# Optimization experiments

Measured on AMD Instinct MI355X. Metric: run time of the kernel, lower is better.

The kernel has to match this reference:

```python
import jax, jax.numpy as jnp
import numpy as np

CONF_THRES = 0.5   # self.conf_thres
NMS_THRES = 0.5    # self.nms_thres
PRE_NMS = 2048     # candidates kept before pairwise IoU
MAX_DET = 300      # padded detections returned per image
MAX_WH = 4096.0    # class-offset trick so NMS is per-class
IMG_SIZE = 416.0   # self.img_size; boxes_scale (416,416)->(416,416) => scale 1


def xywh2xyxy(b):
    xy, wh = b[..., :2], b[..., 2:4]
    return jnp.concatenate([xy - wh * 0.5, xy + wh * 0.5], axis=-1)


def pairwise_iou(boxes):
    # boxes: [K,4] xyxy -> [K,K] IoU
    area = (boxes[:, 2] - boxes[:, 0]) * (boxes[:, 3] - boxes[:, 1])
    lt = jnp.maximum(boxes[:, None, :2], boxes[None, :, :2])
    rb = jnp.minimum(boxes[:, None, 2:], boxes[None, :, 2:])
    wh = jnp.clip(rb - lt, 0.0)
    inter = wh[..., 0] * wh[..., 1]
    return inter / (area[:, None] + area[None, :] - inter + 1e-16)


def nms_single(pred):
    # pred: [N,85] = xywh(4) + objectness(1) + class scores(80)
    boxes = xywh2xyxy(pred[:, :4])
    obj = pred[:, 4]
    cls_scores = pred[:, 5:] * obj[:, None]        # conf = obj * class prob
    conf = jnp.max(cls_scores, axis=-1)
    cls_id = jnp.argmax(cls_scores, axis=-1)
    valid = obj >= CONF_THRES                      # confidence threshold filter
    score = jnp.where(valid, conf, -1.0)

    order = jnp.argsort(-score)[:PRE_NMS]          # sort desc, keep top PRE_NMS
    boxes_s = boxes[order]
    score_s = score[order]
    cls_s = cls_id[order]
    valid_s = valid[order]

    # per-class NMS via coordinate offset by class id
    off = cls_s.astype(boxes_s.dtype) * MAX_WH
    iou = pairwise_iou(boxes_s + off[:, None])     # [PRE_NMS, PRE_NMS]

    def body(keep, i):
        suppressed = jnp.any(keep & (iou[:, i] > NMS_THRES))
        k = valid_s[i] & ~suppressed
        return keep.at[i].set(k), k

    keep, _ = jax.lax.scan(body, jnp.zeros(PRE_NMS, dtype=bool), jnp.arange(PRE_NMS))

    final_score = jnp.where(keep, score_s, -1.0)
    top = jnp.argsort(-final_score)[:MAX_DET]
    kb, ks, kc, km = boxes_s[top], score_s[top], cls_s[top], keep[top]

    scale = IMG_SIZE / 416.0                       # boxes_scale (identity here)
    det = jnp.concatenate(
        [kb * scale, ks[:, None], kc[:, None].astype(kb.dtype)], axis=-1)
    return jnp.where(km[:, None], det, 0.0)        # [MAX_DET, 6] padded


def setup_inputs() -> dict:
    key = jax.random.key(0)
    predictions = jax.random.uniform(key, (16, 10647, 85), dtype=jnp.float32)
    return {"predictions": predictions}


def reference(predictions):
    # detections per image: [x1,y1,x2,y2,score,class], zero-padded to MAX_DET
    return jax.vmap(nms_single)(predictions)  # [B, MAX_DET, 6]
```

## Files before the change

### kernel.cpp

```cpp
#include <hip/hip_runtime.h>
#include <hip/hip_bf16.h>
#include <stdint.h>

typedef unsigned long long u64;
typedef unsigned int u32;
typedef unsigned short u16;

#define NANCH 10647
#define NBATCH 16
#define NSORT 16384
#define NSEL 2048
#define NWORD 32
#define NCLS 80
#define CONF_T 0.5f
#define NMS_T 0.5f
#define MAXDET 300
#define MAXWH 4096.0f
#define CANDCAP 10688
#define PART 1344
#define NBLK1 84

__device__ __forceinline__ float dec_score(u64 key) {
    u32 v = ~(u32)(key >> 32);
    u32 u = (v & 0x80000000u) ? (v & 0x7FFFFFFFu) : ~v;
    return __uint_as_float(u);
}

__global__ __launch_bounds__(256) void k_prep(const float* __restrict__ pred,
                                              u64* __restrict__ keys,
                                              float4* __restrict__ boxes,
                                              int* __restrict__ cls,
                                              u32* __restrict__ bhist) {
    __shared__ float sm[128 * 85];
    __shared__ u32 ph[256];
    int b = blockIdx.y;
    int a0 = blockIdx.x * 128;
    int na = NANCH - a0; if (na > 128) na = 128;
    const float* src = pred + ((size_t)b * NANCH + a0) * 85;
    int tot = na * 85;
    ph[threadIdx.x] = 0;
    {
        size_t srcaddr = (size_t)src;
        int shift = (int)((srcaddr & 15) >> 2);
        const float4* A = (const float4*)(srcaddr & ~(size_t)15);
        int nvec = (tot + shift + 3) >> 2;
        for (int j = threadIdx.x; j < nvec; j += 256) {
            float4 v = A[j];
            int base = 4 * j - shift;
            if (base >= 0 && base + 3 < tot) {
                sm[base] = v.x; sm[base + 1] = v.y;
                sm[base + 2] = v.z; sm[base + 3] = v.w;
            } else {
                if (base >= 0 && base < tot)         sm[base]     = v.x;
                if (base + 1 >= 0 && base + 1 < tot) sm[base + 1] = v.y;
                if (base + 2 >= 0 && base + 2 < tot) sm[base + 2] = v.z;
                if (base + 3 >= 0 && base + 3 < tot) sm[base + 3] = v.w;
            }
        }
    }
    __syncthreads();
    int t = threadIdx.x;
    u64 kk = 0;
    if (t < na) {
        const float* s = &sm[t * 85];
        float x = s[0], y = s[1], w = s[2], h = s[3], obj = s[4];
        float best = s[5] * obj; int arg = 0;
        #pragma unroll
        for (int c = 1; c < 80; ++c) {
            float v = s[5 + c] * obj;
            if (v > best) { best = v; arg = c; }
        }
        bool valid = obj >= CONF_T;
        float sc = valid ? best : -1.0f;
        int a = a0 + t;
        float4 bx;
        bx.x = x - w * 0.5f; bx.y = y - h * 0.5f;
        bx.z = x + w * 0.5f; bx.w = y + h * 0.5f;
        size_t o = (size_t)b * NANCH + a;
        boxes[o] = bx;
        cls[o] = arg;
        u32 u = __float_as_uint(sc);
        u32 v = (u & 0x80000000u) ? ~u : (u | 0x80000000u);
        u32 hi = ~v;
        kk = ((u64)hi << 32) | (u32)a;
        keys[(size_t)b * NSORT + a] = kk;
    }
    u32 bin = (t < na) ? (u32)(kk >> 56) : 0xFFFFFFFFu;
    int lane = t & 63;
    u64 rem = __ballot(t < na);
    while (rem) {
        int srcl = __ffsll((long long)rem) - 1;
        u32 lb = __shfl(bin, srcl);
        u64 same = __ballot(bin == lb) & rem;
        if (lane == srcl) atomicAdd(&ph[lb], (u32)__popcll(same));
        rem &= ~same;
    }
    __syncthreads();
    bhist[(((size_t)b * NBLK1) + blockIdx.x) * 256 + threadIdx.x] = ph[threadIdx.x];
}

__global__ __launch_bounds__(1024) void k_scan(const u64* __restrict__ keys,
                                               const u32* __restrict__ bhist,
                                               u64* __restrict__ gslice,
                                               uint2* __restrict__ gpart) {
    __shared__ u32 hist[256];
    __shared__ u32 hsc[256];
    __shared__ u32 s_D0;
    __shared__ u32 wcs[16], wcc[16];
    __shared__ u32 s_tc;
    int b = blockIdx.y;
    int part = blockIdx.x;
    int tid = threadIdx.x;
    int lane = tid & 63, wv = tid >> 6;
    u64 below = (1ULL << lane) - 1ULL;
    const u64* KB = keys + (size_t)b * NSORT;

    if (tid < 256) {
        u32 h = 0;
        const u32* BH = bhist + (size_t)b * NBLK1 * 256 + tid;
        for (int j = 0; j < NBLK1; ++j) h += BH[(size_t)j * 256];
        hist[tid] = h;
    }
    __syncthreads();
    if (tid < 64) {
        u32 h0 = hist[tid*4], h1 = hist[tid*4+1], h2 = hist[tid*4+2], h3 = hist[tid*4+3];
        u32 loc = h0 + h1 + h2 + h3;
        u32 p = loc;
        #pragma unroll
        for (int o = 1; o < 64; o <<= 1) { u32 t2 = __shfl_up(p, o); if (lane >= o) p += t2; }
        u32 base = p - loc;
        hsc[tid*4]   = base + h0;
        hsc[tid*4+1] = base + h0 + h1;
        hsc[tid*4+2] = base + h0 + h1 + h2;
        hsc[tid*4+3] = base + h0 + h1 + h2 + h3;
    }
    __syncthreads();
    if (tid < 256) {
        u32 inc = hsc[tid], cb = inc - hist[tid];
        if (cb < NSEL && NSEL <= inc) s_D0 = tid;
    }
    __syncthreads();
    u32 D0 = s_D0;

    u64 kk0 = 0, kk1 = 0;
    bool s0 = false, s1 = false, c0 = false, c1 = false;
    {
        int off = tid, i = part * PART + off;
        bool inb = (off < PART) && (i < NANCH);
        kk0 = inb ? KB[i] : 0ULL;
        u32 top = (u32)(kk0 >> 56);
        s0 = inb && (top < D0); c0 = inb && (top == D0);
    }
    {
        int off = 1024 + tid, i = part * PART + off;
        bool inb = (off < PART) && (i < NANCH);
        kk1 = inb ? KB[i] : 0ULL;
        u32 top = (u32)(kk1 >> 56);
        s1 = inb && (top < D0); c1 = inb && (top == D0);
    }
    u64 bs0 = __ballot(s0), bs1 = __ballot(s1);
    u64 bc0 = __ballot(c0), bc1 = __ballot(c1);
    if (lane == 0) {
        wcs[wv] = (u32)(__popcll(bs0) + __popcll(bs1));
        wcc[wv] = (u32)(__popcll(bc0) + __popcll(bc1));
    }
    __syncthreads();
    if (tid < 16) {
        u32 vs = wcs[tid], vc = wcc[tid];
        u32 ps = vs, pc = vc;
        #pragma unroll
        for (int o = 1; o < 16; o <<= 1) {
            u32 ts = __shfl_up(ps, o);
            u32 tc = __shfl_up(pc, o);
            if (tid >= o) { ps += ts; pc += tc; }
        }
        wcs[tid] = ps - vs;
        wcc[tid] = pc - vc;
        if (tid == 15) {
            s_tc = pc;
            gpart[(size_t)b * 8 + part] = make_uint2(ps, pc);
        }
    }
    __syncthreads();
    u64* SL = gslice + ((size_t)b * 8 + part) * (size_t)PART;
    u32 base_s = wcs[wv];
    u32 base_c = (u32)PART - s_tc + wcc[wv];
    if (s0) SL[base_s + __popcll(bs0 & below)] = kk0;
    if (s1) SL[base_s + __popcll(bs0) + __popcll(bs1 & below)] = kk1;
    if (c0) SL[base_c + __popcll(bc0 & below)] = kk0;
    if (c1) SL[base_c + __popcll(bc0) + __popcll(bc1 & below)] = kk1;
}

__global__ __launch_bounds__(1024) void k_fin(const u64* __restrict__ gslice,
                                              const uint2* __restrict__ gpart,
                                              u64* __restrict__ gskey,
                                              u64* __restrict__ gkeep) {
    __shared__ u64 sk[NSEL];
    __shared__ u64 cand[CANDCAP];
    __shared__ u32 hist[256];
    __shared__ u32 hsc[256];
    __shared__ u64 s_red[16];
    __shared__ u32 ssA[8], ccA[8], soff[9], coff[9];
    __shared__ u32 s_D, s_rank, s_cnt, s_cand;

    int b = blockIdx.x;
    int tid = threadIdx.x;
    int lane = tid & 63;
    u64 below = (1ULL << lane) - 1ULL;

    if (tid < 8) { uint2 v = gpart[(size_t)b * 8 + tid]; ssA[tid] = v.x; ccA[tid] = v.y; }
    for (int i = tid; i < NSEL; i += 1024) sk[i] = ~0ULL;
    __syncthreads();
    if (tid == 0) {
        u32 a = 0, c2 = 0;
        for (int j = 0; j < 8; ++j) { soff[j] = a; a += ssA[j]; coff[j] = c2; c2 += ccA[j]; }
        soff[8] = a; coff[8] = c2;
        s_cnt = a; s_rank = NSEL - a; s_cand = c2;
    }
    __syncthreads();
    for (int j = 0; j < 8; ++j) {
        const u64* SL = gslice + ((size_t)b * 8 + j) * (size_t)PART;
        u32 ns = ssA[j], nc = ccA[j];
        u32 so = soff[j], co = coff[j];
        for (u32 i = tid; i < ns; i += 1024) sk[so + i] = SL[i];
        for (u32 i = tid; i < nc; i += 1024) cand[co + i] = SL[PART - nc + i];
    }
    __syncthreads();

    const int shifts2[5] = {48, 40, 32, 8, 0};
    for (int rr = 0; ; ++rr) {
        u32 cn = s_cand, r = s_rank;
        if (r == cn || rr == 5) {
            for (u32 i0 = 0; i0 < cn; i0 += 1024) {
                u32 i = i0 + tid;
                bool take = i < cn;
                u64 kk = take ? cand[i] : 0ULL;
                u64 bt = __ballot(take);
                u32 base = 0;
                if (lane == 0 && bt) base = atomicAdd(&s_cnt, (u32)__popcll(bt));
                base = __shfl(base, 0);
                if (take) sk[base + __popcll(bt & below)] = kk;
            }
            break;
        }
        if (r == 1) {
            u64 best = ~0ULL;
            for (u32 i = tid; i < cn; i += 1024) { u64 kk = cand[i]; if (kk < best) best = kk; }
            #pragma unroll
            for (int o = 32; o > 0; o >>= 1) {
                u64 other = __shfl_down(best, o);
                if (other < best) best = other;
            }
            if (lane == 0) s_red[tid >> 6] = best;
            __syncthreads();
            if (tid == 0) {
                u64 m = s_red[0];
                for (int w2 = 1; w2 < 16; ++w2) if (s_red[w2] < m) m = s_red[w2];
                sk[atomicAdd(&s_cnt, 1u)] = m;
            }
            break;
        }
        int shift = shifts2[rr];
        if (tid < 256) hist[tid] = 0;
        __syncthreads();
        for (u32 i = tid; i < cn; i += 1024)
            atomicAdd(&hist[(u32)(cand[i] >> shift) & 0xFFu], 1u);
        __syncthreads();
        if (tid < 64) {
            u32 h0 = hist[tid*4], h1 = hist[tid*4+1], h2 = hist[tid*4+2], h3 = hist[tid*4+3];
            u32 loc = h0 + h1 + h2 + h3;
            u32 p = loc;
            #pragma unroll
            for (int o = 1; o < 64; o <<= 1) { u32 t2 = __shfl_up(p, o); if (lane >= o) p += t2; }
            u32 base = p - loc;
            hsc[tid*4]   = base + h0;
            hsc[tid*4+1] = base + h0 + h1;
            hsc[tid*4+2] = base + h0 + h1 + h2;
            hsc[tid*4+3] = base + h0 + h1 + h2 + h3;
        }
        __syncthreads();
        if (tid < 256) {
            u32 inc = hsc[tid], cb = inc - hist[tid];
            if (cb < r && r <= inc) { s_D = tid; s_rank = r - cb; }
        }
        __syncthreads();
        u32 D = s_D;
        u64 vv[11]; bool vb[11];
        #pragma unroll
        for (int it = 0; it < 11; ++it) {
            u32 i = tid + it * 1024;
            vb[it] = (i < cn);
            vv[it] = vb[it] ? cand[i] : 0ULL;
        }
        __syncthreads();
        if (tid == 0) s_cand = 0;
        __syncthreads();
        #pragma unroll
        for (int it = 0; it < 11; ++it) {
            u32 dg = (u32)(vv[it] >> shift) & 0xFFu;
            bool tk = vb[it] && (dg < D);
            u64 bt = __ballot(tk);
            u32 base = 0;
            if (lane == 0 && bt) base = atomicAdd(&s_cnt, (u32)__popcll(bt));
            base = __shfl(base, 0);
            if (tk) sk[base + __popcll(bt & below)] = vv[it];
        }
        #pragma unroll
        for (int it = 0; it < 11; ++it) {
            u32 dg = (u32)(vv[it] >> shift) & 0xFFu;
            bool tk = vb[it] && (dg == D);
            u64 bt = __ballot(tk);
            u32 base = 0;
            if (lane == 0 && bt) base = atomicAdd(&s_cand, (u32)__popcll(bt));
            base = __shfl(base, 0);
            if (tk) cand[base + __popcll(bt & below)] = vv[it];
        }
        __syncthreads();
    }
    __syncthreads();

    {
        int w = tid >> 6, l = lane;
        int base = w * 128;
        u64 a = sk[base + l], c = sk[base + 64 + l];
        #pragma unroll
        for (int k = 2; k <= 128; k <<= 1) {
            for (int j = k >> 1; j > 0; j >>= 1) {
                if (j == 64) {
                    bool dir = (((base + l) & k) == 0);
                    u64 lo = a < c ? a : c;
                    u64 hi = a < c ? c : a;
                    a = dir ? lo : hi;
                    c = dir ? hi : lo;
                } else {
                    bool up_ = (l & j) != 0;
                    bool dira = (((base + l) & k) == 0);
                    bool dirc = (((base + 64 + l) & k) == 0);
                    u64 pa = __shfl_xor(a, j);
                    u64 pc = __shfl_xor(c, j);
                    a = (up_ == dira) ? (a > pa ? a : pa) : (a < pa ? a : pa);
                    c = (up_ == dirc) ? (c > pc ? c : pc) : (c < pc ? c : pc);
                }
            }
        }
        sk[base + l] = a; sk[base + 64 + l] = c;
        __syncthreads();
        for (int k = 256; k <= NSEL; k <<= 1) {
            for (int j = k >> 1; j >= 128; j >>= 1) {
                int n = tid;
                int i = ((n & ~(j - 1)) << 1) | (n & (j - 1));
                int l2 = i | j;
                u64 x = sk[i], y = sk[l2];
                bool up2 = ((i & k) == 0);
                if ((x > y) == up2) { sk[i] = y; sk[l2] = x; }
                __syncthreads();
            }
            a = sk[base + l]; c = sk[base + 64 + l];
            bool dirk = ((base & k) == 0);
            {
                u64 lo = a < c ? a : c;
                u64 hi = a < c ? c : a;
                a = dirk ? lo : hi;
                c = dirk ? hi : lo;
            }
            #pragma unroll
            for (int j = 32; j > 0; j >>= 1) {
                bool up_ = (l & j) != 0;
                u64 pa = __shfl_xor(a, j);
                u64 pc = __shfl_xor(c, j);
                a = (up_ == dirk) ? (a > pa ? a : pa) : (a < pa ? a : pa);
                c = (up_ == dirk) ? (c > pc ? c : pc) : (c < pc ? c : pc);
            }
            sk[base + l] = a; sk[base + 64 + l] = c;
            __syncthreads();
        }
    }

    for (int i = tid; i < NSEL; i += 1024) gskey[(size_t)b * NSEL + i] = sk[i];
    if (tid < NWORD) gkeep[(size_t)b * NWORD + tid] = 0ULL;
}

__global__ __launch_bounds__(256) void k_gather(const u64* __restrict__ gskey,
                                                const float4* __restrict__ boxes,
                                                const int* __restrict__ cls,
                                                float4* __restrict__ sel_box,
                                                float4* __restrict__ sel_sbox,
                                                float* __restrict__ sel_area,
                                                float* __restrict__ sel_score,
                                                int* __restrict__ sel_cls) {
    int b = blockIdx.y;
    int r = blockIdx.x * 256 + threadIdx.x;
    u64 key = gskey[(size_t)b * NSEL + r];
    int a = (int)(key & 0xFFFFFFFFu);
    if ((unsigned)a >= NANCH) a = 0;
    size_t src = (size_t)b * NANCH + a;
    float4 bx = boxes[src];
    int c = cls[src];
    float sc = dec_score(key);
    float off = (float)c * MAXWH;
    float4 sb;
    sb.x = bx.x + off; sb.y = bx.y + off;
    sb.z = bx.z + off; sb.w = bx.w + off;
    float area = (sb.z - sb.x) * (sb.w - sb.y);
    size_t o = (size_t)b * NSEL + r;
    sel_box[o] = bx; sel_sbox[o] = sb; sel_area[o] = area;
    sel_score[o] = sc; sel_cls[o] = c;
}

__global__ __launch_bounds__(1024) void k_cnms(const float4* __restrict__ sel_sbox,
                                               const float* __restrict__ sel_area,
                                               const int* __restrict__ sel_cls,
                                               const float* __restrict__ sel_score,
                                               u64* __restrict__ gkeep) {
    __shared__ u16 wmem[16][NSEL];
    __shared__ u64 wkeep[16][NWORD];

    int b = blockIdx.y;
    int cg = blockIdx.x;
    int lane = threadIdx.x & 63, wv = threadIdx.x >> 6;
    int c = cg * 16 + wv;
    size_t bb = (size_t)b * NSEL;
    const int* CL = sel_cls + bb;
    const float* SC = sel_score + bb;
    u64 below = (1ULL << lane) - 1ULL;

    int n = 0;
    for (int ch = 0; ch < NWORD; ++ch) {
        int i = ch * 64 + lane;
        bool pred = (CL[i] == c) && (SC[i] >= 0.0f);
        u64 bal = __ballot(pred);
        if (pred) wmem[wv][n + __popcll(bal & below)] = (u16)i;
        n += __popcll(bal);
    }

    for (int c0 = 0; c0 < n; c0 += 64) {
        int chunkn = n - c0; if (chunkn > 64) chunkn = 64;
        bool mv = lane < chunkn;
        int q = mv ? (int)wmem[wv][c0 + lane] : 0;
        float4 bq = sel_sbox[bb + q];
        float aq = sel_area[bb + q];

        bool hit = false;
        for (int j = 0; j < c0; ++j) {
            if (!((wkeep[wv][j >> 6] >> (j & 63)) & 1ULL)) continue;
            int p = (int)wmem[wv][j];
            float4 bp = sel_sbox[bb + p];
            float ap = sel_area[bb + p];
            float ltx = fmaxf(bp.x, bq.x), lty = fmaxf(bp.y, bq.y);
            float rbx = fminf(bp.z, bq.z), rby = fminf(bp.w, bq.w);
            float ww = fmaxf(rbx - ltx, 0.0f), hh = fmaxf(rby - lty, 0.0f);
            float inter = ww * hh;
            hit = hit || (mv && (inter / (ap + aq - inter + 1e-16f) > NMS_T));
        }
        u64 avail = __ballot(mv && !hit);

        u64 Rt = 0;
        for (int t = 0; t < chunkn; ++t) {
            int p = (int)wmem[wv][c0 + t];
            float4 bp = sel_sbox[bb + p];
            float ap = sel_area[bb + p];
            float ltx = fmaxf(bp.x, bq.x), lty = fmaxf(bp.y, bq.y);
            float rbx = fminf(bp.z, bq.z), rby = fminf(bp.w, bq.w);
            float ww = fmaxf(rbx - ltx, 0.0f), hh = fmaxf(rby - lty, 0.0f);
            float inter = ww * hh;
            u64 row = __ballot(mv && (inter / (ap + aq - inter + 1e-16f) > NMS_T));
            if (lane == t) Rt = row;
        }

        u64 U = avail, kept = 0;
        while (U) {
            bool inU = ((U >> lane) & 1ULL) != 0ULL;
            u64 newk = __ballot(inU && ((Rt & U & below) == 0ULL));
            u64 killed = __ballot((Rt & newk) != 0ULL);
            kept |= newk;
            U &= ~(newk | killed);
        }
        if (lane == 0) wkeep[wv][c0 >> 6] = kept;
        if ((kept >> lane) & 1ULL)
            atomicOr(&gkeep[(size_t)b * NWORD + (q >> 6)], 1ULL << (q & 63));
    }
}

__global__ __launch_bounds__(64) void k_out(const u64* __restrict__ gkeep,
                                            const float4* __restrict__ sel_box,
                                            const float* __restrict__ sel_score,
                                            const int* __restrict__ sel_cls,
                                            float* __restrict__ out) {
    int b = blockIdx.x;
    int lane = threadIdx.x;
    const float* SC = sel_score + (size_t)b * NSEL;
    u64 kreg = (lane < NWORD) ? gkeep[(size_t)b * NWORD + lane] : 0ULL;

    int cnt = (lane < NWORD) ? __popcll(kreg) : 0;
    int pre = cnt;
    #pragma unroll
    for (int dd = 1; dd < 64; dd <<= 1) {
        int o = __shfl_up(pre, dd);
        if (lane >= dd) pre += o;
    }
    int total = __shfl(pre, 63);
    int base = pre - cnt;
    float* OUT = out + (size_t)b * MAXDET * 6;
    if (lane < NWORD) {
        u64 m = kreg;
        int rr = 0;
        while (m) {
            int t = __ffsll((long long)m) - 1;
            m &= m - 1;
            int slot = base + rr; ++rr;
            if (slot < MAXDET) {
                int i = lane * 64 + t;
                size_t src = (size_t)b * NSEL + i;
                float4 bx = sel_box[src];
                float sc = SC[i];
                int c = sel_cls[src];
                float* o6 = OUT + slot * 6;
                o6[0] = bx.x; o6[1] = bx.y; o6[2] = bx.z; o6[3] = bx.w;
                o6[4] = sc; o6[5] = (float)c;
            }
        }
    }
    int start = total > MAXDET ? MAXDET : total;
    for (int s = start + lane; s < MAXDET; s += 64) {
        float* o6 = OUT + s * 6;
        o6[0] = 0.0f; o6[1] = 0.0f; o6[2] = 0.0f;
        o6[3] = 0.0f; o6[4] = 0.0f; o6[5] = 0.0f;
    }
}

extern "C" void kernel_launch(void* const* d_in, const int* in_sizes, int n_in,
                              void* d_out, int out_size, void* d_ws, size_t ws_size,
                              hipStream_t stream) {
    const float* pred = (const float*)d_in[0];
    float* out = (float*)d_out;

    char* ws = (char*)d_ws;
    size_t off = 0;
    auto alloc = [&](size_t bytes) -> void* {
        void* p = ws + off;
        off += (bytes + 255) & ~(size_t)255;
        return p;
    };

    u64*    keys      = (u64*)   alloc((size_t)NBATCH * NSORT * 8);
    float4* boxes     = (float4*)alloc((size_t)NBATCH * NANCH * 16);
    int*    cls       = (int*)   alloc((size_t)NBATCH * NANCH * 4);
    u32*    bhist     = (u32*)   alloc((size_t)NBATCH * NBLK1 * 256 * 4);
    u64*    gslice    = (u64*)   alloc((size_t)NBATCH * 8 * PART * 8);
    uint2*  gpart     = (uint2*) alloc((size_t)NBATCH * 8 * 8);
    u64*    gskey     = (u64*)   alloc((size_t)NBATCH * NSEL * 8);
    u64*    gkeep     = (u64*)   alloc((size_t)NBATCH * NWORD * 8);
    float4* sel_box   = (float4*)alloc((size_t)NBATCH * NSEL * 16);
    float4* sel_sbox  = (float4*)alloc((size_t)NBATCH * NSEL * 16);
    float*  sel_area  = (float*) alloc((size_t)NBATCH * NSEL * 4);
    float*  sel_score = (float*) alloc((size_t)NBATCH * NSEL * 4);
    int*    sel_cls   = (int*)   alloc((size_t)NBATCH * NSEL * 4);

    dim3 g1(NBLK1, NBATCH);
    k_prep<<<g1, 256, 0, stream>>>(pred, keys, boxes, cls, bhist);

    dim3 g2(8, NBATCH);
    k_scan<<<g2, 1024, 0, stream>>>(keys, bhist, gslice, gpart);

    k_fin<<<NBATCH, 1024, 0, stream>>>(gslice, gpart, gskey, gkeep);

    dim3 g4(8, NBATCH);
    k_gather<<<g4, 256, 0, stream>>>(gskey, boxes, cls,
                                     sel_box, sel_sbox, sel_area,
                                     sel_score, sel_cls);

    dim3 g5(5, NBATCH);
    k_cnms<<<g5, 1024, 0, stream>>>(sel_sbox, sel_area, sel_cls, sel_score, gkeep);

    k_out<<<NBATCH, 64, 0, stream>>>(gkeep, sel_box, sel_score, sel_cls, out);
}
```

Before: 103.0 us.

## Fuse second radix-select digit histogram into scan kernel and parallelize slice compaction

The scan kernel now also builds a histogram of the second key byte for the boundary-bucket candidates and accumulates it globally with atomics, zeroed in the prep kernel. The final kernel uses that histogram to resolve the second digit up front, so its first radix refinement round over the candidates is skipped. Slice copying is also spread across waves, with one wave per slice for selected keys and one per slice for candidates, using atomic offsets instead of serial per-slice loops. The cost is extra shared and global atomics in the scan kernel, and zeroing ghist2 in k_prep relies on kernel ordering on the stream.

```diff
diff --git a/kernel.cpp b/kernel.cpp
--- a/kernel.cpp
+++ b/kernel.cpp
@@ -30,10 +30,12 @@
                                               u64* __restrict__ keys,
                                               float4* __restrict__ boxes,
                                               int* __restrict__ cls,
-                                              u32* __restrict__ bhist) {
+                                              u32* __restrict__ bhist,
+                                              u32* __restrict__ ghist2) {
     __shared__ float sm[128 * 85];
     __shared__ u32 ph[256];
     int b = blockIdx.y;
+    if (blockIdx.x == 0) ghist2[(size_t)b * 256 + threadIdx.x] = 0;
     int a0 = blockIdx.x * 128;
     int na = NANCH - a0; if (na > 128) na = 128;
     const float* src = pred + ((size_t)b * NANCH + a0) * 85;
@@ -102,9 +104,11 @@
 __global__ __launch_bounds__(1024) void k_scan(const u64* __restrict__ keys,
                                                const u32* __restrict__ bhist,
                                                u64* __restrict__ gslice,
-                                               uint2* __restrict__ gpart) {
+                                               uint2* __restrict__ gpart,
+                                               u32* __restrict__ ghist2) {
     __shared__ u32 hist[256];
     __shared__ u32 hsc[256];
+    __shared__ u32 ph2[256];
     __shared__ u32 s_D0;
     __shared__ u32 wcs[16], wcc[16];
     __shared__ u32 s_tc;
@@ -116,6 +120,7 @@
     const u64* KB = keys + (size_t)b * NSORT;
 
     if (tid < 256) {
+        ph2[tid] = 0;
         u32 h = 0;
         const u32* BH = bhist + (size_t)b * NBLK1 * 256 + tid;
         for (int j = 0; j < NBLK1; ++j) h += BH[(size_t)j * 256];
@@ -158,6 +163,8 @@
         u32 top = (u32)(kk1 >> 56);
         s1 = inb && (top < D0); c1 = inb && (top == D0);
     }
+    if (c0) atomicAdd(&ph2[(u32)(kk0 >> 48) & 0xFFu], 1u);
+    if (c1) atomicAdd(&ph2[(u32)(kk1 >> 48) & 0xFFu], 1u);
     u64 bs0 = __ballot(s0), bs1 = __ballot(s1);
     u64 bc0 = __ballot(c0), bc1 = __ballot(c1);
     if (lane == 0) {
@@ -189,10 +196,12 @@
     if (s1) SL[base_s + __popcll(bs0) + __popcll(bs1 & below)] = kk1;
     if (c0) SL[base_c + __popcll(bc0 & below)] = kk0;
     if (c1) SL[base_c + __popcll(bc0) + __popcll(bc1 & below)] = kk1;
+    if (tid < 256 && ph2[tid]) atomicAdd(&ghist2[(size_t)b * 256 + tid], ph2[tid]);
 }
 
 __global__ __launch_bounds__(1024) void k_fin(const u64* __restrict__ gslice,
                                               const uint2* __restrict__ gpart,
+                                              const u32* __restrict__ ghist2,
                                               u64* __restrict__ gskey,
                                               u64* __restrict__ gkeep) {
     __shared__ u64 sk[NSEL];
@@ -200,35 +209,87 @@
     __shared__ u32 hist[256];
     __shared__ u32 hsc[256];
     __shared__ u64 s_red[16];
-    __shared__ u32 ssA[8], ccA[8], soff[9], coff[9];
-    __shared__ u32 s_D, s_rank, s_cnt, s_cand;
+    __shared__ u32 ssA[8], ccA[8];
+    __shared__ u32 s_D, s_r0, s_rank, s_cnt, s_cand;
 
     int b = blockIdx.x;
     int tid = threadIdx.x;
-    int lane = tid & 63;
+    int lane = tid & 63, wv = tid >> 6;
     u64 below = (1ULL << lane) - 1ULL;
 
     if (tid < 8) { uint2 v = gpart[(size_t)b * 8 + tid]; ssA[tid] = v.x; ccA[tid] = v.y; }
+    if (tid < 256) hist[tid] = ghist2[(size_t)b * 256 + tid];
     for (int i = tid; i < NSEL; i += 1024) sk[i] = ~0ULL;
     __syncthreads();
     if (tid == 0) {
-        u32 a = 0, c2 = 0;
-        for (int j = 0; j < 8; ++j) { soff[j] = a; a += ssA[j]; coff[j] = c2; c2 += ccA[j]; }
-        soff[8] = a; coff[8] = c2;
-        s_cnt = a; s_rank = NSEL - a; s_cand = c2;
-    }
-    __syncthreads();
-    for (int j = 0; j < 8; ++j) {
+        u32 a = 0;
+        for (int j = 0; j < 8; ++j) a += ssA[j];
+        s_r0 = NSEL - a;
+        s_cnt = 0; s_cand = 0;
+    }
+    if (tid < 64) {
+        u32 h0 = hist[tid*4], h1 = hist[tid*4+1], h2 = hist[tid*4+2], h3 = hist[tid*4+3];
+        u32 loc = h0 + h1 + h2 + h3;
+        u32 p = loc;
+        #pragma unroll
+        for (int o = 1; o < 64; o <<= 1) { u32 t2 = __shfl_up(p, o); if (lane >= o) p += t2; }
+        u32 base = p - loc;
+        hsc[tid*4]   = base + h0;
+        hsc[tid*4+1] = base + h0 + h1;
+        hsc[tid*4+2] = base + h0 + h1 + h2;
+        hsc[tid*4+3] = base + h0 + h1 + h2 + h3;
+    }
+    __syncthreads();
+    if (tid < 256) {
+        u32 inc = hsc[tid], cb = inc - hist[tid];
+        u32 r0 = s_r0;
+        if (cb < r0 && r0 <= inc) s_D = tid;
+    }
+    __syncthreads();
+    u32 D48 = s_D;
+
+    if (wv < 8) {
+        int j = wv;
         const u64* SL = gslice + ((size_t)b * 8 + j) * (size_t)PART;
-        u32 ns = ssA[j], nc = ccA[j];
-        u32 so = soff[j], co = coff[j];
-        for (u32 i = tid; i < ns; i += 1024) sk[so + i] = SL[i];
-        for (u32 i = tid; i < nc; i += 1024) cand[co + i] = SL[PART - nc + i];
-    }
+        u32 ns = ssA[j];
+        for (u32 i0 = 0; i0 < ns; i0 += 64) {
+            u32 i = i0 + lane;
+            bool act = i < ns;
+            u64 kk = act ? SL[i] : 0ULL;
+            u64 bal = __ballot(act);
+            u32 base = 0;
+            if (lane == 0) base = atomicAdd(&s_cnt, (u32)__popcll(bal));
+            base = __shfl(base, 0);
+            if (act) sk[base + __popcll(bal & below)] = kk;
+        }
+    } else {
+        int j = wv - 8;
+        u32 nc = ccA[j];
+        const u64* SL = gslice + ((size_t)b * 8 + j) * (size_t)PART + (PART - nc);
+        for (u32 i0 = 0; i0 < nc; i0 += 64) {
+            u32 i = i0 + lane;
+            bool act = i < nc;
+            u64 kk = act ? SL[i] : 0ULL;
+            u32 dg = (u32)(kk >> 48) & 0xFFu;
+            bool tks = act && (dg < D48);
+            bool tkc = act && (dg == D48);
+            u64 bs = __ballot(tks), bc = __ballot(tkc);
+            u32 base_s = 0, base_c = 0;
+            if (lane == 0) {
+                if (bs) base_s = atomicAdd(&s_cnt, (u32)__popcll(bs));
+                if (bc) base_c = atomicAdd(&s_cand, (u32)__popcll(bc));
+            }
+            base_s = __shfl(base_s, 0); base_c = __shfl(base_c, 0);
+            if (tks) sk[base_s + __popcll(bs & below)] = kk;
+            if (tkc) cand[base_c + __popcll(bc & below)] = kk;
+        }
+    }
+    __syncthreads();
+    if (tid == 0) s_rank = NSEL - s_cnt;
     __syncthreads();
 
     const int shifts2[5] = {48, 40, 32, 8, 0};
-    for (int rr = 0; ; ++rr) {
+    for (int rr = 1; ; ++rr) {
         u32 cn = s_cand, r = s_rank;
         if (r == cn || rr == 5) {
             for (u32 i0 = 0; i0 < cn; i0 += 1024) {
@@ -546,6 +607,7 @@
     float4* boxes     = (float4*)alloc((size_t)NBATCH * NANCH * 16);
     int*    cls       = (int*)   alloc((size_t)NBATCH * NANCH * 4);
     u32*    bhist     = (u32*)   alloc((size_t)NBATCH * NBLK1 * 256 * 4);
+    u32*    ghist2    = (u32*)   alloc((size_t)NBATCH * 256 * 4);
     u64*    gslice    = (u64*)   alloc((size_t)NBATCH * 8 * PART * 8);
     uint2*  gpart     = (uint2*) alloc((size_t)NBATCH * 8 * 8);
     u64*    gskey     = (u64*)   alloc((size_t)NBATCH * NSEL * 8);
@@ -557,12 +619,12 @@
     int*    sel_cls   = (int*)   alloc((size_t)NBATCH * NSEL * 4);
 
     dim3 g1(NBLK1, NBATCH);
-    k_prep<<<g1, 256, 0, stream>>>(pred, keys, boxes, cls, bhist);
+    k_prep<<<g1, 256, 0, stream>>>(pred, keys, boxes, cls, bhist, ghist2);
 
     dim3 g2(8, NBATCH);
-    k_scan<<<g2, 1024, 0, stream>>>(keys, bhist, gslice, gpart);
-
-    k_fin<<<NBATCH, 1024, 0, stream>>>(gslice, gpart, gskey, gkeep);
+    k_scan<<<g2, 1024, 0, stream>>>(keys, bhist, gslice, gpart, ghist2);
+
+    k_fin<<<NBATCH, 1024, 0, stream>>>(gslice, gpart, ghist2, gskey, gkeep);
 
     dim3 g4(8, NBATCH);
     k_gather<<<g4, 256, 0, stream>>>(gskey, boxes, cls,
```

Measured after the change: 100.5 us, median of 2. 2.4% less time.
